# Optimization experiments

Hardware: AMD Instinct MI355X
Metric: run time of the kernel (lower is better)

## Reference

```python
import jax, jax.numpy as jnp
import numpy as np

B, T, N, D, K, H = 32, 24, 2048, 64, 32, 16  # batch, timesteps, nodes, dim_in=dim_out, embed_dim, HT_Tem


def setup_inputs() -> dict:
    key = jax.random.key(0)
    ks = jax.random.split(key, 6)
    return {
        "eb": jax.random.normal(ks[0], (B, T, N, D), dtype=jnp.float32),
        "node_embeddings": jax.random.normal(ks[1], (N, K), dtype=jnp.float32),
        "time_eb": jax.random.normal(ks[2], (B, T, K), dtype=jnp.float32),
        "adj": jax.random.normal(ks[3], (K, H, T), dtype=jnp.float32),
        "weights_pool": jax.random.normal(ks[4], (K, D, D), dtype=jnp.float32),
        "bias_pool": jax.random.normal(ks[5], (K, D), dtype=jnp.float32),
    }


def reference(eb, node_embeddings, time_eb, adj, weights_pool, bias_pool):
    # adj_dynamics: [H, T, N] (torch computes nht then permutes to htn)
    adj_dyn = jnp.einsum('nk,kht->htn', node_embeddings, adj)
    # hypergraph aggregation: [B, H, N, D]
    hyper = jnp.einsum('htn,btnd->bhnd', adj_dyn, eb)
    # de-aggregation back to time axis: [B, T, N, D]
    ret = jnp.einsum('htn,bhnd->btnd', adj_dyn, hyper)
    # per-(b,t) generated weights [B, T, D, D] and bias [B, T, 1, D]
    weights = jnp.einsum('btd,dio->btio', time_eb, weights_pool)
    bias = jnp.einsum('btd,do->bto', time_eb, bias_pool)[:, :, None, :]
    out = jnp.einsum('btni,btio->btno', ret, weights) + bias
    return jax.nn.leaky_relu(out + eb, negative_slope=0.01)
```

## Files before the change

kernel.cpp:

```cpp
#include <hip/hip_runtime.h>

#define B_ 32
#define T_ 24
#define N_ 2048
#define D_ 64
#define K_ 32
#define H_ 16
#define NB 16

typedef __attribute__((ext_vector_type(8))) short bf16x8;
typedef __attribute__((ext_vector_type(4))) float f32x4;

__device__ __forceinline__ unsigned short f2bf(float f) {
    unsigned int u = __float_as_uint(f);
    return (unsigned short)((u + 0x7FFFu + ((u >> 16) & 1u)) >> 16);
}
__device__ __forceinline__ float bf2f(unsigned short h) {
    return __uint_as_float(((unsigned int)h) << 16);
}

__global__ void k_prepM(const float* __restrict__ ne, const float* __restrict__ adj,
                        float* __restrict__ M2) {
    __shared__ float s_ne[K_];
    __shared__ float s_ad[H_ * T_];
    const int n = blockIdx.x;
    const int tid = threadIdx.x;
    if (tid < K_) s_ne[tid] = ne[n * K_ + tid];
    __syncthreads();
    for (int f = tid; f < H_ * T_; f += 64) {
        const int h = f / T_, t = f % T_;
        float a = 0.f;
#pragma unroll
        for (int k = 0; k < K_; ++k) a += s_ne[k] * adj[(k * H_ + h) * T_ + t];
        s_ad[f] = a;
    }
    __syncthreads();
    float* dst = M2 + (size_t)(n >> 4) * (T_ * T_ * 16) + (n & 15);
    for (int m = tid; m < T_ * T_; m += 64) {
        const int t = m / T_, t2 = m % T_;
        float a = 0.f;
#pragma unroll
        for (int h = 0; h < H_; ++h) a += s_ad[h * T_ + t] * s_ad[h * T_ + t2];
        dst[m * 16] = a;
    }
}

__global__ __launch_bounds__(256) void k_prepW(const float* __restrict__ te,
                                               const float* __restrict__ wp,
                                               const float* __restrict__ bp,
                                               unsigned short* __restrict__ Wt,
                                               float* __restrict__ bias) {
    const int bt = blockIdx.x;
    const int tid = threadIdx.x;
    __shared__ float s_te[K_];
    __shared__ float s_W[D_ * D_];
    if (tid < K_) s_te[tid] = te[bt * K_ + tid];
    __syncthreads();
    float4 acc[4] = {};
    for (int k = 0; k < K_; ++k) {
        const float tk = s_te[k];
        const float4* row = (const float4*)(wp + (size_t)k * (D_ * D_));
#pragma unroll
        for (int i = 0; i < 4; ++i) {
            float4 v = row[tid + i * 256];
            acc[i].x += tk * v.x; acc[i].y += tk * v.y;
            acc[i].z += tk * v.z; acc[i].w += tk * v.w;
        }
    }
    float4* sW4 = (float4*)s_W;
#pragma unroll
    for (int i = 0; i < 4; ++i) sW4[tid + i * 256] = acc[i];
    if (tid < D_) {
        float a = 0.f;
#pragma unroll
        for (int k = 0; k < K_; ++k) a += s_te[k] * bp[k * D_ + tid];
        bias[bt * D_ + tid] = a;
    }
    __syncthreads();
    const int o = tid >> 2;
    const int i0 = (tid & 3) * 16;
    unsigned short* dst = Wt + (size_t)bt * (D_ * D_) + o * D_ + i0;
#pragma unroll
    for (int j = 0; j < 16; j += 4) {
        ushort4 u;
        u.x = f2bf(s_W[(i0 + j + 0) * D_ + o]);
        u.y = f2bf(s_W[(i0 + j + 1) * D_ + o]);
        u.z = f2bf(s_W[(i0 + j + 2) * D_ + o]);
        u.w = f2bf(s_W[(i0 + j + 3) * D_ + o]);
        *(ushort4*)(dst + j) = u;
    }
}

__global__ __launch_bounds__(512, 4) void k_fused(const float* __restrict__ eb,
                                                  const float* __restrict__ M2,
                                                  const unsigned short* __restrict__ Wt,
                                                  const float* __restrict__ bias,
                                                  float* __restrict__ out) {
    const int b = blockIdx.y;
    const int nb = blockIdx.x * NB;
    const int tid = threadIdx.x;
    const int wave = tid >> 6, lane = tid & 63;
    const int lr = lane & 15, lh = lane >> 4;

    __shared__ unsigned short s_eb[T_ * NB * D_];

    {
        const float* ebb = eb + (size_t)(b * T_) * N_ * D_;
#pragma unroll
        for (int it = 0; it < 12; ++it) {
            const int f4 = it * 512 + tid;
            const int t = f4 >> 8;
            const int n = (f4 >> 4) & 15;
            const int d0 = (f4 & 15) * 4;
            const float4 v = *(const float4*)(ebb + ((size_t)t * N_ + nb + n) * D_ + d0);
            ushort4 u;
            u.x = f2bf(v.x); u.y = f2bf(v.y); u.z = f2bf(v.z); u.w = f2bf(v.w);
            const int inrow = (d0 * 2) ^ ((n & 7) << 4);
            *(ushort4*)((char*)s_eb + t * (NB * 128) + n * 128 + inrow) = u;
        }
    }
    __syncthreads();

    const float* Mblk = M2 + (size_t)blockIdx.x * (T_ * T_ * 16) + lr;
    const char* ebase = (const char*)s_eb;
    const int sw = (lr & 7) << 4;

    const int tb = wave * 3;
    float acc[3][16];
#pragma unroll
    for (int tt = 0; tt < 3; ++tt)
#pragma unroll
        for (int j = 0; j < 16; ++j) acc[tt][j] = 0.f;

#pragma unroll 4
    for (int tp = 0; tp < T_; ++tp) {
        const float* mcol = Mblk + ((size_t)tb * T_ + tp) * 16;
        const float m0 = mcol[0 * T_ * 16];
        const float m1 = mcol[1 * T_ * 16];
        const float m2 = mcol[2 * T_ * 16];
        const char* rowp = ebase + (tp * NB + lr) * 128;
        const bf16x8 e0 = *(const bf16x8*)(rowp + ((lh * 16) ^ sw));
        const bf16x8 e1 = *(const bf16x8*)(rowp + (((lh + 4) * 16) ^ sw));
        float ef[16];
#pragma unroll
        for (int j = 0; j < 8; ++j) {
            ef[j]     = bf2f((unsigned short)e0[j]);
            ef[8 + j] = bf2f((unsigned short)e1[j]);
        }
#pragma unroll
        for (int j = 0; j < 16; ++j) {
            acc[0][j] += m0 * ef[j];
            acc[1][j] += m1 * ef[j];
            acc[2][j] += m2 * ef[j];
        }
    }

    bf16x8 Af[3][2];
#pragma unroll
    for (int tt = 0; tt < 3; ++tt)
#pragma unroll
        for (int j = 0; j < 8; ++j) {
            Af[tt][0][j] = (short)f2bf(acc[tt][j]);
            Af[tt][1][j] = (short)f2bf(acc[tt][8 + j]);
        }

#pragma unroll
    for (int tt = 0; tt < 3; ++tt) {
        const int t = tb + tt;
        const int bt = b * T_ + t;
        const unsigned short* Wb = Wt + (size_t)bt * (D_ * D_);
        f32x4 C[4] = {};
#pragma unroll
        for (int ot = 0; ot < 4; ++ot) {
            const bf16x8 B0 = *(const bf16x8*)(Wb + (ot * 16 + lr) * D_ + lh * 8);
            const bf16x8 B1 = *(const bf16x8*)(Wb + (ot * 16 + lr) * D_ + 32 + lh * 8);
            C[ot] = __builtin_amdgcn_mfma_f32_16x16x32_bf16(Af[tt][0], B0, C[ot], 0, 0, 0);
            C[ot] = __builtin_amdgcn_mfma_f32_16x16x32_bf16(Af[tt][1], B1, C[ot], 0, 0, 0);
        }
        float bv[4];
#pragma unroll
        for (int ot = 0; ot < 4; ++ot) bv[ot] = bias[bt * D_ + ot * 16 + lr];

        float* obt = out + ((size_t)bt * N_ + nb) * D_;
#pragma unroll
        for (int r = 0; r < 4; ++r) {
            const int nn = lh * 4 + r;
            const char* erow = ebase + (t * NB + nn) * 128;
            const int swn = (nn & 7) << 4;
#pragma unroll
            for (int ot = 0; ot < 4; ++ot) {
                const int o = ot * 16 + lr;
                const unsigned short eu =
                    *(const unsigned short*)(erow + ((o * 2) ^ swn));
                float v = C[ot][r] + bv[ot] + bf2f(eu);
                v = v >= 0.f ? v : 0.01f * v;
                obt[(size_t)nn * D_ + o] = v;
            }
        }
    }
}

extern "C" void kernel_launch(void* const* d_in, const int* in_sizes, int n_in,
                              void* d_out, int out_size, void* d_ws, size_t ws_size,
                              hipStream_t stream) {
    const float* eb  = (const float*)d_in[0];
    const float* ne  = (const float*)d_in[1];
    const float* te  = (const float*)d_in[2];
    const float* adj = (const float*)d_in[3];
    const float* wp  = (const float*)d_in[4];
    const float* bp  = (const float*)d_in[5];
    float* out = (float*)d_out;

    char* ws = (char*)d_ws;
    const size_t M_bytes  = (size_t)N_ * T_ * T_ * 4;
    const size_t Wt_bytes = (size_t)B_ * T_ * D_ * D_ * 2;
    float* M2          = (float*)ws;
    unsigned short* Wt = (unsigned short*)(ws + M_bytes);
    float* bias        = (float*)(ws + M_bytes + Wt_bytes);

    k_prepM<<<N_, 64, 0, stream>>>(ne, adj, M2);
    k_prepW<<<B_ * T_, 256, 0, stream>>>(te, wp, bp, Wt, bias);
    k_fused<<<dim3(N_ / NB, B_), 512, 0, stream>>>(eb, M2, Wt, bias, out);
}
```

Baseline: 297.7 us.

## Store mixing matrix in bf16 and stage it through shared memory

The T×T per-node mixing matrix M2 is now stored in bf16 in a node-major layout, which halves its workspace footprint and global traffic. The fused kernel loads its block's slice into a padded LDS buffer once, and each thread then pulls its three rows as vector loads. This replaces the scalar global loads issued inside the time loop. The time loop is fully unrolled by a macro, at the cost of extra bf16 rounding of M and more registers and LDS per block.

```diff
diff --git a/kernel.cpp b/kernel.cpp
--- a/kernel.cpp
+++ b/kernel.cpp
@@ -20,7 +20,7 @@
 }
 
 __global__ void k_prepM(const float* __restrict__ ne, const float* __restrict__ adj,
-                        float* __restrict__ M2) {
+                        unsigned short* __restrict__ M2) {
     __shared__ float s_ne[K_];
     __shared__ float s_ad[H_ * T_];
     const int n = blockIdx.x;
@@ -35,13 +35,13 @@
         s_ad[f] = a;
     }
     __syncthreads();
-    float* dst = M2 + (size_t)(n >> 4) * (T_ * T_ * 16) + (n & 15);
+    unsigned short* dst = M2 + (size_t)(n >> 4) * (T_ * T_ * 16) + (n & 15) * T_;
     for (int m = tid; m < T_ * T_; m += 64) {
         const int t = m / T_, t2 = m % T_;
         float a = 0.f;
 #pragma unroll
         for (int h = 0; h < H_; ++h) a += s_ad[h * T_ + t] * s_ad[h * T_ + t2];
-        dst[m * 16] = a;
+        dst[t * (16 * T_) + t2] = f2bf(a);
     }
 }
 
@@ -91,8 +91,27 @@
     }
 }
 
+#define MIXC(MV0, MV1, MV2, CB)                                        \
+    _Pragma("unroll")                                                  \
+    for (int j = 0; j < 8; ++j) {                                      \
+        const int tp = (CB) + j;                                       \
+        const bf16x8 e0 = *(const bf16x8*)(base0 + tp * 2048);         \
+        const bf16x8 e1 = *(const bf16x8*)(base1 + tp * 2048);         \
+        const float f0 = bf2f((unsigned short)MV0[j]);                 \
+        const float f1 = bf2f((unsigned short)MV1[j]);                 \
+        const float f2 = bf2f((unsigned short)MV2[j]);                 \
+        _Pragma("unroll")                                              \
+        for (int q = 0; q < 8; ++q) {                                  \
+            const float ea = bf2f((unsigned short)e0[q]);              \
+            const float eb2 = bf2f((unsigned short)e1[q]);             \
+            acc[0][q] += f0 * ea; acc[0][8 + q] += f0 * eb2;           \
+            acc[1][q] += f1 * ea; acc[1][8 + q] += f1 * eb2;           \
+            acc[2][q] += f2 * ea; acc[2][8 + q] += f2 * eb2;           \
+        }                                                              \
+    }
+
 __global__ __launch_bounds__(512, 4) void k_fused(const float* __restrict__ eb,
-                                                  const float* __restrict__ M2,
+                                                  const unsigned short* __restrict__ M2,
                                                   const unsigned short* __restrict__ Wt,
                                                   const float* __restrict__ bias,
                                                   float* __restrict__ out) {
@@ -103,6 +122,7 @@
     const int lr = lane & 15, lh = lane >> 4;
 
     __shared__ unsigned short s_eb[T_ * NB * D_];
+    __shared__ unsigned short s_M[T_ * NB * 26];
 
     {
         const float* ebb = eb + (size_t)(b * T_) * N_ * D_;
@@ -119,41 +139,47 @@
             *(ushort4*)((char*)s_eb + t * (NB * 128) + n * 128 + inrow) = u;
         }
     }
-    __syncthreads();
-
-    const float* Mblk = M2 + (size_t)blockIdx.x * (T_ * T_ * 16) + lr;
+    {
+        const unsigned short* Mblk = M2 + (size_t)blockIdx.x * (T_ * T_ * 16);
+#pragma unroll
+        for (int it = 0; it < 18; ++it) {
+            const int e = it * 512 + tid;
+            const int t = e / (16 * T_);
+            const int rem = e - t * (16 * T_);
+            const int n = rem / T_;
+            const int tp = rem - n * T_;
+            s_M[(t * 16 + n) * 26 + tp] = Mblk[e];
+        }
+    }
+    __syncthreads();
+
     const char* ebase = (const char*)s_eb;
     const int sw = (lr & 7) << 4;
-
     const int tb = wave * 3;
+
+    const char* mbase = (const char*)s_M + (tb * 16 + lr) * 52;
+    const bf16x8 m0c0 = *(const bf16x8*)(mbase + 0 * 832 + 0);
+    const bf16x8 m0c1 = *(const bf16x8*)(mbase + 0 * 832 + 16);
+    const bf16x8 m0c2 = *(const bf16x8*)(mbase + 0 * 832 + 32);
+    const bf16x8 m1c0 = *(const bf16x8*)(mbase + 1 * 832 + 0);
+    const bf16x8 m1c1 = *(const bf16x8*)(mbase + 1 * 832 + 16);
+    const bf16x8 m1c2 = *(const bf16x8*)(mbase + 1 * 832 + 32);
+    const bf16x8 m2c0 = *(const bf16x8*)(mbase + 2 * 832 + 0);
+    const bf16x8 m2c1 = *(const bf16x8*)(mbase + 2 * 832 + 16);
+    const bf16x8 m2c2 = *(const bf16x8*)(mbase + 2 * 832 + 32);
+
+    const char* base0 = ebase + lr * 128 + ((lh * 16) ^ sw);
+    const char* base1 = ebase + lr * 128 + ((((lh + 4) * 16)) ^ sw);
+
     float acc[3][16];
 #pragma unroll
     for (int tt = 0; tt < 3; ++tt)
 #pragma unroll
         for (int j = 0; j < 16; ++j) acc[tt][j] = 0.f;
 
-#pragma unroll 4
-    for (int tp = 0; tp < T_; ++tp) {
-        const float* mcol = Mblk + ((size_t)tb * T_ + tp) * 16;
-        const float m0 = mcol[0 * T_ * 16];
-        const float m1 = mcol[1 * T_ * 16];
-        const float m2 = mcol[2 * T_ * 16];
-        const char* rowp = ebase + (tp * NB + lr) * 128;
-        const bf16x8 e0 = *(const bf16x8*)(rowp + ((lh * 16) ^ sw));
-        const bf16x8 e1 = *(const bf16x8*)(rowp + (((lh + 4) * 16) ^ sw));
-        float ef[16];
-#pragma unroll
-        for (int j = 0; j < 8; ++j) {
-            ef[j]     = bf2f((unsigned short)e0[j]);
-            ef[8 + j] = bf2f((unsigned short)e1[j]);
-        }
-#pragma unroll
-        for (int j = 0; j < 16; ++j) {
-            acc[0][j] += m0 * ef[j];
-            acc[1][j] += m1 * ef[j];
-            acc[2][j] += m2 * ef[j];
-        }
-    }
+    MIXC(m0c0, m1c0, m2c0, 0)
+    MIXC(m0c1, m1c1, m2c1, 8)
+    MIXC(m0c2, m1c2, m2c2, 16)
 
     bf16x8 Af[3][2];
 #pragma unroll
@@ -212,9 +238,9 @@
     float* out = (float*)d_out;
 
     char* ws = (char*)d_ws;
-    const size_t M_bytes  = (size_t)N_ * T_ * T_ * 4;
+    const size_t M_bytes  = (size_t)N_ * T_ * T_ * 2;
     const size_t Wt_bytes = (size_t)B_ * T_ * D_ * D_ * 2;
-    float* M2          = (float*)ws;
+    unsigned short* M2 = (unsigned short*)ws;
     unsigned short* Wt = (unsigned short*)(ws + M_bytes);
     float* bias        = (float*)(ws + M_bytes + Wt_bytes);
 
```

New measurement: 920.3 us. +209.1%, slower.

## Store mixing matrix as bf16 and stage it in shared memory per block

Applied to the files above, without the earlier changes.

The precomputed T×T node mixing matrix is now stored in bf16 with a node-major layout. Each block stages its 16-node slice into shared memory once, instead of every wave issuing scattered fp32 global loads inside the time loop. The inner loop is fully unrolled with hoisted LDS base pointers, and the occupancy hint in launch bounds is lowered to 2. This cuts global traffic and load latency in the aggregation loop, at the cost of extra LDS, lower occupancy and reduced precision in the mixing coefficients.

```diff
diff --git a/kernel.cpp b/kernel.cpp
--- a/kernel.cpp
+++ b/kernel.cpp
@@ -20,7 +20,7 @@
 }
 
 __global__ void k_prepM(const float* __restrict__ ne, const float* __restrict__ adj,
-                        float* __restrict__ M2) {
+                        unsigned short* __restrict__ M2) {
     __shared__ float s_ne[K_];
     __shared__ float s_ad[H_ * T_];
     const int n = blockIdx.x;
@@ -35,13 +35,13 @@
         s_ad[f] = a;
     }
     __syncthreads();
-    float* dst = M2 + (size_t)(n >> 4) * (T_ * T_ * 16) + (n & 15);
+    unsigned short* dst = M2 + (size_t)(n >> 4) * (T_ * T_ * 16) + (n & 15) * T_;
     for (int m = tid; m < T_ * T_; m += 64) {
         const int t = m / T_, t2 = m % T_;
         float a = 0.f;
 #pragma unroll
         for (int h = 0; h < H_; ++h) a += s_ad[h * T_ + t] * s_ad[h * T_ + t2];
-        dst[m * 16] = a;
+        dst[t * (16 * T_) + t2] = f2bf(a);
     }
 }
 
@@ -91,8 +91,8 @@
     }
 }
 
-__global__ __launch_bounds__(512, 4) void k_fused(const float* __restrict__ eb,
-                                                  const float* __restrict__ M2,
+__global__ __launch_bounds__(512, 2) void k_fused(const float* __restrict__ eb,
+                                                  const unsigned short* __restrict__ M2,
                                                   const unsigned short* __restrict__ Wt,
                                                   const float* __restrict__ bias,
                                                   float* __restrict__ out) {
@@ -103,6 +103,7 @@
     const int lr = lane & 15, lh = lane >> 4;
 
     __shared__ unsigned short s_eb[T_ * NB * D_];
+    __shared__ unsigned short s_M[T_ * NB * T_];
 
     {
         const float* ebb = eb + (size_t)(b * T_) * N_ * D_;
@@ -119,39 +120,44 @@
             *(ushort4*)((char*)s_eb + t * (NB * 128) + n * 128 + inrow) = u;
         }
     }
-    __syncthreads();
-
-    const float* Mblk = M2 + (size_t)blockIdx.x * (T_ * T_ * 16) + lr;
+    {
+        const unsigned short* Mblk = M2 + (size_t)blockIdx.x * (T_ * T_ * 16);
+#pragma unroll
+        for (int it = 0; it < 18; ++it) {
+            const int e = it * 512 + tid;
+            s_M[e] = Mblk[e];
+        }
+    }
+    __syncthreads();
+
     const char* ebase = (const char*)s_eb;
     const int sw = (lr & 7) << 4;
-
     const int tb = wave * 3;
+
+    const unsigned short* mrow = s_M + tb * (16 * T_) + lr * T_;
+    const char* base0 = ebase + lr * 128 + ((lh * 16) ^ sw);
+    const char* base1 = ebase + lr * 128 + ((((lh + 4) * 16)) ^ sw);
+
     float acc[3][16];
 #pragma unroll
     for (int tt = 0; tt < 3; ++tt)
 #pragma unroll
         for (int j = 0; j < 16; ++j) acc[tt][j] = 0.f;
 
-#pragma unroll 4
+#pragma unroll
     for (int tp = 0; tp < T_; ++tp) {
-        const float* mcol = Mblk + ((size_t)tb * T_ + tp) * 16;
-        const float m0 = mcol[0 * T_ * 16];
-        const float m1 = mcol[1 * T_ * 16];
-        const float m2 = mcol[2 * T_ * 16];
-        const char* rowp = ebase + (tp * NB + lr) * 128;
-        const bf16x8 e0 = *(const bf16x8*)(rowp + ((lh * 16) ^ sw));
-        const bf16x8 e1 = *(const bf16x8*)(rowp + (((lh + 4) * 16) ^ sw));
-        float ef[16];
-#pragma unroll
-        for (int j = 0; j < 8; ++j) {
-            ef[j]     = bf2f((unsigned short)e0[j]);
-            ef[8 + j] = bf2f((unsigned short)e1[j]);
-        }
-#pragma unroll
-        for (int j = 0; j < 16; ++j) {
-            acc[0][j] += m0 * ef[j];
-            acc[1][j] += m1 * ef[j];
-            acc[2][j] += m2 * ef[j];
+        const float m0 = bf2f(mrow[tp]);
+        const float m1 = bf2f(mrow[384 + tp]);
+        const float m2 = bf2f(mrow[768 + tp]);
+        const bf16x8 e0 = *(const bf16x8*)(base0 + tp * 2048);
+        const bf16x8 e1 = *(const bf16x8*)(base1 + tp * 2048);
+#pragma unroll
+        for (int q = 0; q < 8; ++q) {
+            const float ea = bf2f((unsigned short)e0[q]);
+            const float eb2 = bf2f((unsigned short)e1[q]);
+            acc[0][q] += m0 * ea; acc[0][8 + q] += m0 * eb2;
+            acc[1][q] += m1 * ea; acc[1][8 + q] += m1 * eb2;
+            acc[2][q] += m2 * ea; acc[2][8 + q] += m2 * eb2;
         }
     }
 
@@ -212,9 +218,9 @@
     float* out = (float*)d_out;
 
     char* ws = (char*)d_ws;
-    const size_t M_bytes  = (size_t)N_ * T_ * T_ * 4;
+    const size_t M_bytes  = (size_t)N_ * T_ * T_ * 2;
     const size_t Wt_bytes = (size_t)B_ * T_ * D_ * D_ * 2;
-    float* M2          = (float*)ws;
+    unsigned short* M2 = (unsigned short*)ws;
     unsigned short* Wt = (unsigned short*)(ws + M_bytes);
     float* bias        = (float*)(ws + M_bytes + Wt_bytes);
 
```

Result: faster. 284.6 us (-4.4%).

## Pipeline eb tile loads with temporal mixing in chunks of eight timesteps

Applied to the files above, without the earlier changes.

Splits the shared-memory staging of the eb tile into three chunks of 8 timesteps. The global loads for the next chunk are issued before the mixing FMAs over the current chunk, so memory latency overlaps with compute instead of the whole block waiting on one big load phase. Launch bounds drop from 4 to 2 blocks per SM, which gives the extra register-held prefetch buffers room but may lower occupancy.

```diff
diff --git a/kernel.cpp b/kernel.cpp
--- a/kernel.cpp
+++ b/kernel.cpp
@@ -91,69 +91,94 @@
     }
 }
 
-__global__ __launch_bounds__(512, 4) void k_fused(const float* __restrict__ eb,
+#define EBLD(F, C, GV)                                                      \
+    {                                                                       \
+        const int f_ = (F);                                                 \
+        const int t_ = ((C) * 8) + (f_ >> 8);                               \
+        const int rem_ = f_ & 255;                                          \
+        const int n_ = rem_ >> 4;                                           \
+        const int d0_ = (rem_ & 15) * 4;                                    \
+        GV = *(const float4*)(ebb + ((size_t)t_ * N_ + nb + n_) * D_ + d0_);\
+    }
+#define EBST(F, C, GV)                                                      \
+    {                                                                       \
+        const int f_ = (F);                                                 \
+        const int t_ = ((C) * 8) + (f_ >> 8);                               \
+        const int rem_ = f_ & 255;                                          \
+        const int n_ = rem_ >> 4;                                           \
+        const int d0_ = (rem_ & 15) * 4;                                    \
+        ushort4 u_;                                                         \
+        u_.x = f2bf(GV.x); u_.y = f2bf(GV.y);                               \
+        u_.z = f2bf(GV.z); u_.w = f2bf(GV.w);                               \
+        *(ushort4*)((char*)s_eb + t_ * 2048 + n_ * 128 +                    \
+                    ((d0_ * 2) ^ ((n_ & 7) << 4))) = u_;                    \
+    }
+#define MIXCHUNK(C)                                                         \
+    _Pragma("unroll")                                                       \
+    for (int tpl = 0; tpl < 8; ++tpl) {                                     \
+        const int tp = (C) * 8 + tpl;                                       \
+        const float m0 = Mb[((tb + 0) * T_ + tp) * 16];                     \
+        const float m1 = Mb[((tb + 1) * T_ + tp) * 16];                     \
+        const float m2 = Mb[((tb + 2) * T_ + tp) * 16];                     \
+        const char* rowp = ebase + (tp * NB + lr) * 128;                    \
+        const bf16x8 e0 = *(const bf16x8*)(rowp + ((lh * 16) ^ sw));        \
+        const bf16x8 e1 = *(const bf16x8*)(rowp + (((lh + 4) * 16) ^ sw));  \
+        float ef[16];                                                       \
+        _Pragma("unroll")                                                   \
+        for (int j = 0; j < 8; ++j) {                                       \
+            ef[j] = bf2f((unsigned short)e0[j]);                            \
+            ef[8 + j] = bf2f((unsigned short)e1[j]);                        \
+        }                                                                   \
+        _Pragma("unroll")                                                   \
+        for (int j = 0; j < 16; ++j) {                                      \
+            acc[0][j] += m0 * ef[j];                                        \
+            acc[1][j] += m1 * ef[j];                                        \
+            acc[2][j] += m2 * ef[j];                                        \
+        }                                                                   \
+    }
+
+__global__ __launch_bounds__(512, 2) void k_fused(const float* __restrict__ eb,
                                                   const float* __restrict__ M2,
                                                   const unsigned short* __restrict__ Wt,
                                                   const float* __restrict__ bias,
                                                   float* __restrict__ out) {
     const int b = blockIdx.y;
-    const int nb = blockIdx.x * NB;
+    const int nbI = blockIdx.x;
+    const int nb = nbI * NB;
     const int tid = threadIdx.x;
     const int wave = tid >> 6, lane = tid & 63;
     const int lr = lane & 15, lh = lane >> 4;
 
     __shared__ unsigned short s_eb[T_ * NB * D_];
 
-    {
-        const float* ebb = eb + (size_t)(b * T_) * N_ * D_;
-#pragma unroll
-        for (int it = 0; it < 12; ++it) {
-            const int f4 = it * 512 + tid;
-            const int t = f4 >> 8;
-            const int n = (f4 >> 4) & 15;
-            const int d0 = (f4 & 15) * 4;
-            const float4 v = *(const float4*)(ebb + ((size_t)t * N_ + nb + n) * D_ + d0);
-            ushort4 u;
-            u.x = f2bf(v.x); u.y = f2bf(v.y); u.z = f2bf(v.z); u.w = f2bf(v.w);
-            const int inrow = (d0 * 2) ^ ((n & 7) << 4);
-            *(ushort4*)((char*)s_eb + t * (NB * 128) + n * 128 + inrow) = u;
-        }
-    }
-    __syncthreads();
-
-    const float* Mblk = M2 + (size_t)blockIdx.x * (T_ * T_ * 16) + lr;
+    const float* ebb = eb + (size_t)(b * T_) * N_ * D_;
+    const float* Mb = M2 + (size_t)nbI * (T_ * T_ * 16) + lr;
     const char* ebase = (const char*)s_eb;
     const int sw = (lr & 7) << 4;
-
     const int tb = wave * 3;
+
     float acc[3][16];
 #pragma unroll
     for (int tt = 0; tt < 3; ++tt)
 #pragma unroll
         for (int j = 0; j < 16; ++j) acc[tt][j] = 0.f;
 
-#pragma unroll 4
-    for (int tp = 0; tp < T_; ++tp) {
-        const float* mcol = Mblk + ((size_t)tb * T_ + tp) * 16;
-        const float m0 = mcol[0 * T_ * 16];
-        const float m1 = mcol[1 * T_ * 16];
-        const float m2 = mcol[2 * T_ * 16];
-        const char* rowp = ebase + (tp * NB + lr) * 128;
-        const bf16x8 e0 = *(const bf16x8*)(rowp + ((lh * 16) ^ sw));
-        const bf16x8 e1 = *(const bf16x8*)(rowp + (((lh + 4) * 16) ^ sw));
-        float ef[16];
-#pragma unroll
-        for (int j = 0; j < 8; ++j) {
-            ef[j]     = bf2f((unsigned short)e0[j]);
-            ef[8 + j] = bf2f((unsigned short)e1[j]);
-        }
-#pragma unroll
-        for (int j = 0; j < 16; ++j) {
-            acc[0][j] += m0 * ef[j];
-            acc[1][j] += m1 * ef[j];
-            acc[2][j] += m2 * ef[j];
-        }
-    }
+    float4 g0, g1, g2, g3;
+    EBLD(tid, 0, g0) EBLD(tid + 512, 0, g1) EBLD(tid + 1024, 0, g2) EBLD(tid + 1536, 0, g3)
+    EBST(tid, 0, g0) EBST(tid + 512, 0, g1) EBST(tid + 1024, 0, g2) EBST(tid + 1536, 0, g3)
+    __syncthreads();
+
+    EBLD(tid, 1, g0) EBLD(tid + 512, 1, g1) EBLD(tid + 1024, 1, g2) EBLD(tid + 1536, 1, g3)
+    MIXCHUNK(0)
+    EBST(tid, 1, g0) EBST(tid + 512, 1, g1) EBST(tid + 1024, 1, g2) EBST(tid + 1536, 1, g3)
+    __syncthreads();
+
+    EBLD(tid, 2, g0) EBLD(tid + 512, 2, g1) EBLD(tid + 1024, 2, g2) EBLD(tid + 1536, 2, g3)
+    MIXCHUNK(1)
+    EBST(tid, 2, g0) EBST(tid + 512, 2, g1) EBST(tid + 1024, 2, g2) EBST(tid + 1536, 2, g3)
+    __syncthreads();
+
+    MIXCHUNK(2)
 
     bf16x8 Af[3][2];
 #pragma unroll
```

After: 298.0 us. Within noise of the previous version (+0.1%).
